# Optimization experiments

Hardware: AMD Instinct MI355X
Metric: run time of the kernel (lower is better)

The kernel has to match this reference:

```python
import jax, jax.numpy as jnp
import numpy as np

B, S, D = 2, 2048, 1024
N_HEADS = 16
HEAD_DIM = D // N_HEADS
D_FF = 4 * D
EPS = 1e-5


def setup_inputs() -> dict:
    key = jax.random.key(0)
    ks = jax.random.split(key, 16)
    s = 0.02
    return {
        "x": jax.random.normal(ks[0], (B, S, D), dtype=jnp.float32),
        "ln1_scale": jnp.ones((D,), jnp.float32),
        "ln1_shift": jnp.zeros((D,), jnp.float32),
        "wq": jax.random.normal(ks[1], (D, D), jnp.float32) * s,
        "wk": jax.random.normal(ks[2], (D, D), jnp.float32) * s,
        "wv": jax.random.normal(ks[3], (D, D), jnp.float32) * s,
        "wo": jax.random.normal(ks[4], (D, D), jnp.float32) * s,
        "bo": jnp.zeros((D,), jnp.float32),
        "ln2_scale": jnp.ones((D,), jnp.float32),
        "ln2_shift": jnp.zeros((D,), jnp.float32),
        "w1": jax.random.normal(ks[5], (D, D_FF), jnp.float32) * s,
        "b1": jnp.zeros((D_FF,), jnp.float32),
        "w2": jax.random.normal(ks[6], (D_FF, D), jnp.float32) * s,
        "b2": jnp.zeros((D,), jnp.float32),
    }


def _layer_norm(x, scale, shift):
    mean = jnp.mean(x, axis=-1, keepdims=True)
    var = jnp.var(x, axis=-1, keepdims=True)  # unbiased=False
    return (x - mean) / jnp.sqrt(var + EPS) * scale + shift


def _mha(x, wq, wk, wv, wo, bo):
    b, s, d = x.shape
    q = (x @ wq).reshape(b, s, N_HEADS, HEAD_DIM).transpose(0, 2, 1, 3)
    k = (x @ wk).reshape(b, s, N_HEADS, HEAD_DIM).transpose(0, 2, 1, 3)
    v = (x @ wv).reshape(b, s, N_HEADS, HEAD_DIM).transpose(0, 2, 1, 3)
    scores = jnp.einsum('bhqd,bhkd->bhqk', q, k)
    causal = jnp.tril(jnp.ones((s, s), dtype=bool))  # mask upper triangle
    scores = jnp.where(causal, scores, -jnp.inf)
    attn = jax.nn.softmax(scores / np.sqrt(HEAD_DIM).astype(np.float32), axis=-1)
    ctx = jnp.einsum('bhqk,bhkd->bhqd', attn, v)
    ctx = ctx.transpose(0, 2, 1, 3).reshape(b, s, d)
    return ctx @ wo + bo


def reference(x, ln1_scale, ln1_shift, wq, wk, wv, wo, bo,
              ln2_scale, ln2_shift, w1, b1, w2, b2):
    # Attention sub-block (dropout is identity in eval / droprate=0)
    h = x + _mha(_layer_norm(x, ln1_scale, ln1_shift), wq, wk, wv, wo, bo)
    # FFN sub-block (note: original code discards the dropout(inp) result and
    # returns shortcut + ff_output, which is the standard residual)
    y = _layer_norm(h, ln2_scale, ln2_shift)
    ff = jax.nn.gelu(y @ w1 + b1, approximate=True) @ w2 + b2
    return h + ff
```

## Files before the change

### kernel.cpp

```cpp
#include <hip/hip_runtime.h>
#include <hip/hip_bf16.h>

typedef unsigned short u16;
typedef unsigned int u32;
typedef __bf16 bf16x8 __attribute__((ext_vector_type(8)));
typedef float f32x4 __attribute__((ext_vector_type(4)));

#if __has_builtin(__builtin_amdgcn_exp2f)
#define FEXP2 __builtin_amdgcn_exp2f
#else
#define FEXP2 exp2f
#endif

#define QSCALE 0.1803368801f

__device__ __forceinline__ u16 f2bf(float f) {
  __hip_bfloat16 h = __float2bfloat16(f);
  return __builtin_bit_cast(u16, h);
}

__device__ __forceinline__ void load_lds16(const u16* g, u16* l) {
  __builtin_amdgcn_global_load_lds((const __attribute__((address_space(1))) void*)g,
                                   (__attribute__((address_space(3))) void*)l, 16, 0, 0);
}

__global__ __launch_bounds__(256) void tconv_kernel(const float* __restrict__ src,
                                                    u16* __restrict__ dst, int R, int C) {
  __shared__ float tile[32][33];
  int bx = blockIdx.x * 32, by = blockIdx.y * 32;
  int tx = threadIdx.x, ty = threadIdx.y;
#pragma unroll
  for (int i = 0; i < 4; ++i)
    tile[ty + 8 * i][tx] = src[(size_t)(by + ty + 8 * i) * C + bx + tx];
  __syncthreads();
#pragma unroll
  for (int i = 0; i < 4; ++i)
    dst[(size_t)(bx + ty + 8 * i) * R + by + tx] = f2bf(tile[tx][ty + 8 * i]);
}

__global__ __launch_bounds__(256) void ln_kernel(const float* __restrict__ src,
                                                 u16* __restrict__ dst,
                                                 const float* __restrict__ gamma,
                                                 const float* __restrict__ beta) {
  int row = blockIdx.x, tid = threadIdx.x;
  const float4 v = ((const float4*)(src + (size_t)row * 1024))[tid];
  float s = v.x + v.y + v.z + v.w;
  float q = v.x * v.x + v.y * v.y + v.z * v.z + v.w * v.w;
#pragma unroll
  for (int off = 32; off >= 1; off >>= 1) {
    s += __shfl_down(s, off, 64);
    q += __shfl_down(q, off, 64);
  }
  __shared__ float red[8];
  if ((tid & 63) == 0) { red[(tid >> 6) * 2] = s; red[(tid >> 6) * 2 + 1] = q; }
  __syncthreads();
  s = red[0] + red[2] + red[4] + red[6];
  q = red[1] + red[3] + red[5] + red[7];
  float mean = s * (1.0f / 1024.0f);
  float var = q * (1.0f / 1024.0f) - mean * mean;
  float rstd = rsqrtf(var + 1e-5f);
  float4 g = ((const float4*)gamma)[tid];
  float4 b = ((const float4*)beta)[tid];
  ushort4 o;
  o.x = f2bf((v.x - mean) * rstd * g.x + b.x);
  o.y = f2bf((v.y - mean) * rstd * g.y + b.y);
  o.z = f2bf((v.z - mean) * rstd * g.z + b.z);
  o.w = f2bf((v.w - mean) * rstd * g.w + b.w);
  *(ushort4*)(dst + (size_t)row * 1024 + tid * 4) = o;
}

template <int MODE, int BN>
__global__ __launch_bounds__(256) void gemm_st(const u16* __restrict__ A,
                                               const u16* __restrict__ BT,
                                               int M, int N, int K,
                                               const float* __restrict__ bias,
                                               const float* __restrict__ resid,
                                               void* __restrict__ outp,
                                               void* __restrict__ outp2,
                                               void* __restrict__ outp3) {
  constexpr int NJ = BN / 32;
  const int tid = threadIdx.x, lane = tid & 63, wave = tid >> 6;
  const int l16 = lane & 15, quad = lane >> 4;
  const int mblk = blockIdx.y * 128, nblk = blockIdx.x * BN;
  const int m0w = (wave >> 1) * 64, n0w = (wave & 1) * (BN / 2);

  __shared__ u16 Ab[128 * 32];
  __shared__ u16 Bb[BN * 32];

  f32x4 acc[4][NJ];
#pragma unroll
  for (int i = 0; i < 4; ++i)
#pragma unroll
    for (int j = 0; j < NJ; ++j)
#pragma unroll
      for (int r = 0; r < 4; ++r) acc[i][j][r] = 0.0f;

  const int srow = lane >> 2, schunk = lane & 3;
  const u16* gA = A + (size_t)(mblk + wave * 32 + srow) * K + schunk * 8;
  u16* lA = Ab + (wave * 32) * 32;
  const u16* gB;
  u16* lB;
  if constexpr (BN == 128) {
    gB = BT + (size_t)(nblk + wave * 32 + srow) * K + schunk * 8;
    lB = Bb + (wave * 32) * 32;
  } else {
    gB = BT + (size_t)(nblk + wave * 16 + srow) * K + schunk * 8;
    lB = Bb + (wave * 16) * 32;
  }

  for (int k0 = 0; k0 < K; k0 += 32) {
    __syncthreads();
    load_lds16(gA + k0, lA);
    load_lds16(gA + 16 * (size_t)K + k0, lA + 16 * 32);
    if constexpr (BN == 128) {
      load_lds16(gB + k0, lB);
      load_lds16(gB + 16 * (size_t)K + k0, lB + 16 * 32);
    } else {
      load_lds16(gB + k0, lB);
    }
    asm volatile("s_waitcnt vmcnt(0)" ::: "memory");
    __syncthreads();

    bf16x8 af[4], bfr[NJ];
#pragma unroll
    for (int i = 0; i < 4; ++i)
      af[i] = *(const bf16x8*)(Ab + (m0w + i * 16 + l16) * 32 + quad * 8);
#pragma unroll
    for (int j = 0; j < NJ; ++j)
      bfr[j] = *(const bf16x8*)(Bb + (n0w + j * 16 + l16) * 32 + quad * 8);
#pragma unroll
    for (int i = 0; i < 4; ++i)
#pragma unroll
      for (int j = 0; j < NJ; ++j)
        acc[i][j] = __builtin_amdgcn_mfma_f32_16x16x32_bf16(af[i], bfr[j], acc[i][j], 0, 0, 0);
  }

#pragma unroll
  for (int i = 0; i < 4; ++i) {
#pragma unroll
    for (int j = 0; j < NJ; ++j) {
      const int col = nblk + n0w + j * 16 + l16;
#pragma unroll
      for (int r = 0; r < 4; ++r) {
        const int row = mblk + m0w + i * 16 + quad * 4 + r;
        float v = acc[i][j][r];
        if constexpr (MODE == 0) {
          const int slotc = col >> 6;
          const int ty = slotc >> 4;
          const int h = slotc & 15, d = col & 63;
          const int bb = row >> 11, s = row & 2047;
          if (ty == 0) {
            ((u16*)outp)[(((size_t)(bb * 16 + h)) * 2048 + s) * 64 + d] = f2bf(v * QSCALE);
          } else if (ty == 1) {
            ((u16*)outp2)[(((size_t)(bb * 16 + h)) * 2048 + s) * 64 + d] = f2bf(v);
          } else {
            const int spos = (s & ~31) | ((s & 15) << 1) | ((s >> 4) & 1);
            ((u16*)outp3)[(((size_t)(bb * 16 + h)) * 64 + d) * 2048 + spos] = f2bf(v);
          }
        } else if constexpr (MODE == 3) {
          ((float*)outp)[(size_t)row * N + col] = v + bias[col] + resid[(size_t)row * N + col];
        } else if constexpr (MODE == 4) {
          float u = v + bias[col];
          float c = 0.7978845608f * u * (1.0f + 0.044715f * u * u);
          float a = fabsf(c);
          float e = __expf(-2.0f * a);
          float th = (1.0f - e) / (1.0f + e);
          th = copysignf(th, c);
          ((u16*)outp)[(size_t)row * N + col] = f2bf(0.5f * u * (1.0f + th));
        } else if constexpr (MODE == 5) {
          ((float*)outp)[(size_t)row * N + col] =
              v + bias[col] + resid[(size_t)row * N + col];
        }
      }
    }
  }
}

__global__ __launch_bounds__(128) void attn_kernel(const u16* __restrict__ Q,
                                                   const u16* __restrict__ Kb,
                                                   const u16* __restrict__ VT,
                                                   u16* __restrict__ ctx) {
  const int tid = threadIdx.x, lane = tid & 63, wave = tid >> 6;
  const int l16 = lane & 15, quad = lane >> 4;
  const int id = blockIdx.x, xcd = id & 7, slot = id >> 3;
  const int bh = xcd + 8 * (slot & 3);
  const int qt = 31 - (slot >> 2);
  const int b = bh >> 4, hh = bh & 15;
  const int q0 = qt * 64 + wave * 32;

  const u16* qp = Q + (size_t)bh * 2048 * 64;
  const u16* kp = Kb + (size_t)bh * 2048 * 64;
  const u16* vp = VT + (size_t)bh * 64 * 2048;

  bf16x8 qf[2][2];
#pragma unroll
  for (int rf = 0; rf < 2; ++rf)
#pragma unroll
    for (int kk = 0; kk < 2; ++kk)
      qf[rf][kk] = *(const bf16x8*)(qp + (size_t)(q0 + rf * 16 + l16) * 64 + kk * 32 + quad * 8);

  f32x4 o[2][4], lac[2];
#pragma unroll
  for (int rf = 0; rf < 2; ++rf) {
#pragma unroll
    for (int r = 0; r < 4; ++r) lac[rf][r] = 0.0f;
#pragma unroll
    for (int dt = 0; dt < 4; ++dt)
#pragma unroll
      for (int r = 0; r < 4; ++r) o[rf][dt][r] = 0.0f;
  }

  bf16x8 onef;
#pragma unroll
  for (int i = 0; i < 8; ++i) onef[i] = (__bf16)1.0f;

  __shared__ u16 pbuf[2][32 * 40];
  u16* pw = pbuf[wave];

  const int nfull = q0 >> 5;

  bf16x8 kf[2][2], vf[4], kfn[2][2], vfn[4];
#pragma unroll
  for (int st = 0; st < 2; ++st)
#pragma unroll
    for (int kk = 0; kk < 2; ++kk)
      kf[st][kk] = *(const bf16x8*)(kp + (size_t)(st * 16 + l16) * 64 + kk * 32 + quad * 8);
#pragma unroll
  for (int dt = 0; dt < 4; ++dt)
    vf[dt] = *(const bf16x8*)(vp + (size_t)(dt * 16 + l16) * 2048 + quad * 8);

  for (int kt = 0; kt <= nfull; ++kt) {
    const int kb0 = kt * 32;
    f32x4 sc[2][2];
#pragma unroll
    for (int rf = 0; rf < 2; ++rf)
#pragma unroll
      for (int st = 0; st < 2; ++st) {
#pragma unroll
        for (int r = 0; r < 4; ++r) sc[rf][st][r] = 0.0f;
#pragma unroll
        for (int kk = 0; kk < 2; ++kk)
          sc[rf][st] = __builtin_amdgcn_mfma_f32_16x16x32_bf16(qf[rf][kk], kf[st][kk], sc[rf][st], 0, 0, 0);
      }

    const int kbn = (kt < nfull) ? kb0 + 32 : 0;
#pragma unroll
    for (int st = 0; st < 2; ++st)
#pragma unroll
      for (int kk = 0; kk < 2; ++kk)
        kfn[st][kk] = *(const bf16x8*)(kp + (size_t)(kbn + st * 16 + l16) * 64 + kk * 32 + quad * 8);
#pragma unroll
    for (int dt = 0; dt < 4; ++dt)
      vfn[dt] = *(const bf16x8*)(vp + (size_t)(dt * 16 + l16) * 2048 + kbn + quad * 8);

    const bool masked = (kt == nfull);
#pragma unroll
    for (int rf = 0; rf < 2; ++rf)
#pragma unroll
      for (int r = 0; r < 4; ++r) {
        float s0 = sc[rf][0][r], s1 = sc[rf][1][r];
        if (masked) {
          const int rel = rf * 16 + quad * 4 + r;
          if (l16 > rel) s0 = -INFINITY;
          if (16 + l16 > rel) s1 = -INFINITY;
        }
        const u32 pk = (u32)f2bf(FEXP2(s0)) | ((u32)f2bf(FEXP2(s1)) << 16);
        *(u32*)(pw + (rf * 16 + quad * 4 + r) * 40 + l16 * 2) = pk;
      }
    asm volatile("s_waitcnt lgkmcnt(0)" ::: "memory");
#pragma unroll
    for (int rf = 0; rf < 2; ++rf) {
      bf16x8 pf = *(const bf16x8*)(pw + (rf * 16 + l16) * 40 + quad * 8);
      lac[rf] = __builtin_amdgcn_mfma_f32_16x16x32_bf16(pf, onef, lac[rf], 0, 0, 0);
#pragma unroll
      for (int dt = 0; dt < 4; ++dt)
        o[rf][dt] = __builtin_amdgcn_mfma_f32_16x16x32_bf16(pf, vf[dt], o[rf][dt], 0, 0, 0);
    }
#pragma unroll
    for (int st = 0; st < 2; ++st)
#pragma unroll
      for (int kk = 0; kk < 2; ++kk) kf[st][kk] = kfn[st][kk];
#pragma unroll
    for (int dt = 0; dt < 4; ++dt) vf[dt] = vfn[dt];
  }

#pragma unroll
  for (int rf = 0; rf < 2; ++rf)
#pragma unroll
    for (int r = 0; r < 4; ++r) {
      const float inv = 1.0f / lac[rf][r];
      const int row = q0 + rf * 16 + quad * 4 + r;
#pragma unroll
      for (int dt = 0; dt < 4; ++dt) {
        const int col = dt * 16 + l16;
        ctx[((size_t)(b * 2048 + row)) * 1024 + hh * 64 + col] = f2bf(o[rf][dt][r] * inv);
      }
    }
}

extern "C" void kernel_launch(void* const* d_in, const int* in_sizes, int n_in,
                              void* d_out, int out_size, void* d_ws, size_t ws_size,
                              hipStream_t stream) {
  (void)in_sizes; (void)n_in; (void)out_size; (void)ws_size;
  const float* x    = (const float*)d_in[0];
  const float* g1   = (const float*)d_in[1];
  const float* s1   = (const float*)d_in[2];
  const float* wq   = (const float*)d_in[3];
  const float* wk   = (const float*)d_in[4];
  const float* wv   = (const float*)d_in[5];
  const float* wo   = (const float*)d_in[6];
  const float* bo   = (const float*)d_in[7];
  const float* g2   = (const float*)d_in[8];
  const float* s2   = (const float*)d_in[9];
  const float* w1   = (const float*)d_in[10];
  const float* b1   = (const float*)d_in[11];
  const float* w2   = (const float*)d_in[12];
  const float* b2   = (const float*)d_in[13];

  char* ws = (char*)d_ws;
  u16* wqkvT = (u16*)(ws + 0);
  u16* woT   = (u16*)(ws + 6291456);
  u16* w1T   = (u16*)(ws + 8388608);
  u16* w2T   = (u16*)(ws + 16777216);
  u16* xn    = (u16*)(ws + 25165824);
  u16* qb    = (u16*)(ws + 33554432);
  u16* kb    = (u16*)(ws + 41943040);
  u16* vT    = (u16*)(ws + 50331648);
  u16* ctx   = (u16*)(ws + 58720256);
  u16* f     = (u16*)(ws + 33554432);
  float* h   = (float*)(ws + 67108864);
  u16* y     = xn;

  dim3 tb(32, 8);
  tconv_kernel<<<dim3(32, 32), tb, 0, stream>>>(wq, wqkvT, 1024, 1024);
  tconv_kernel<<<dim3(32, 32), tb, 0, stream>>>(wk, wqkvT + 1024 * 1024, 1024, 1024);
  tconv_kernel<<<dim3(32, 32), tb, 0, stream>>>(wv, wqkvT + 2048 * 1024, 1024, 1024);
  tconv_kernel<<<dim3(32, 32), tb, 0, stream>>>(wo, woT, 1024, 1024);
  tconv_kernel<<<dim3(128, 32), tb, 0, stream>>>(w1, w1T, 1024, 4096);
  tconv_kernel<<<dim3(32, 128), tb, 0, stream>>>(w2, w2T, 4096, 1024);

  ln_kernel<<<4096, 256, 0, stream>>>(x, xn, g1, s1);

  gemm_st<0, 128><<<dim3(24, 32), 256, 0, stream>>>(xn, wqkvT, 4096, 3072, 1024,
                                                    nullptr, nullptr, qb, kb, vT);

  attn_kernel<<<1024, 128, 0, stream>>>(qb, kb, vT, ctx);

  gemm_st<3, 64><<<dim3(16, 32), 256, 0, stream>>>(ctx, woT, 4096, 1024, 1024, bo, x, h,
                                                   nullptr, nullptr);

  ln_kernel<<<4096, 256, 0, stream>>>(h, y, g2, s2);

  gemm_st<4, 128><<<dim3(32, 32), 256, 0, stream>>>(y, w1T, 4096, 4096, 1024, b1, nullptr, f,
                                                    nullptr, nullptr);
  gemm_st<5, 64><<<dim3(16, 32), 256, 0, stream>>>(f, w2T, 4096, 1024, 4096, b2, h, (float*)d_out,
                                                   nullptr, nullptr);
}
```

Before: 425.6 us.

## Add XCD-aware block remap and a swizzled K64 GEMM for narrow outputs

All GEMMs now use a 1D grid and remap block ids so each XCD handles a contiguous band of M rows, which should improve L2 reuse of A tiles. The two N=1024 projections (attention output and FFN down) move to a new gemm64 kernel. It uses K-step 64 with XOR-swizzled LDS layout to avoid bank conflicts, halves the barrier count per K, and sets launch bounds for two blocks per SM. Epilogue code is factored into a shared helper. Costs are higher LDS use per block and possible register pressure.

```diff
diff --git a/kernel.cpp b/kernel.cpp
--- a/kernel.cpp
+++ b/kernel.cpp
@@ -69,111 +69,187 @@
   *(ushort4*)(dst + (size_t)row * 1024 + tid * 4) = o;
 }
 
-template <int MODE, int BN>
+template <int MODE>
+__device__ __forceinline__ void epilogue_elem(float v, int row, int col, int N,
+                                              const float* __restrict__ bias,
+                                              const float* __restrict__ resid,
+                                              void* __restrict__ outp,
+                                              void* __restrict__ outp2,
+                                              void* __restrict__ outp3) {
+  if constexpr (MODE == 0) {
+    const int slotc = col >> 6;
+    const int ty = slotc >> 4;
+    const int h = slotc & 15, d = col & 63;
+    const int bb = row >> 11, s = row & 2047;
+    if (ty == 0) {
+      ((u16*)outp)[(((size_t)(bb * 16 + h)) * 2048 + s) * 64 + d] = f2bf(v * QSCALE);
+    } else if (ty == 1) {
+      ((u16*)outp2)[(((size_t)(bb * 16 + h)) * 2048 + s) * 64 + d] = f2bf(v);
+    } else {
+      const int spos = (s & ~31) | ((s & 15) << 1) | ((s >> 4) & 1);
+      ((u16*)outp3)[(((size_t)(bb * 16 + h)) * 64 + d) * 2048 + spos] = f2bf(v);
+    }
+  } else if constexpr (MODE == 3) {
+    ((float*)outp)[(size_t)row * N + col] = v + bias[col] + resid[(size_t)row * N + col];
+  } else if constexpr (MODE == 4) {
+    float u = v + bias[col];
+    float c = 0.7978845608f * u * (1.0f + 0.044715f * u * u);
+    float a = fabsf(c);
+    float e = __expf(-2.0f * a);
+    float th = (1.0f - e) / (1.0f + e);
+    th = copysignf(th, c);
+    ((u16*)outp)[(size_t)row * N + col] = f2bf(0.5f * u * (1.0f + th));
+  } else if constexpr (MODE == 5) {
+    ((float*)outp)[(size_t)row * N + col] = v + bias[col] + resid[(size_t)row * N + col];
+  }
+}
+
+template <int MODE>
 __global__ __launch_bounds__(256) void gemm_st(const u16* __restrict__ A,
                                                const u16* __restrict__ BT,
-                                               int M, int N, int K,
+                                               int M, int N, int K, int nbx,
                                                const float* __restrict__ bias,
                                                const float* __restrict__ resid,
                                                void* __restrict__ outp,
                                                void* __restrict__ outp2,
                                                void* __restrict__ outp3) {
-  constexpr int NJ = BN / 32;
   const int tid = threadIdx.x, lane = tid & 63, wave = tid >> 6;
   const int l16 = lane & 15, quad = lane >> 4;
-  const int mblk = blockIdx.y * 128, nblk = blockIdx.x * BN;
-  const int m0w = (wave >> 1) * 64, n0w = (wave & 1) * (BN / 2);
+  const int id = blockIdx.x, xcd = id & 7, s = id >> 3;
+  const int by = xcd * 4 + s / nbx, bx = s - (s / nbx) * nbx;
+  const int mblk = by * 128, nblk = bx * 128;
+  const int m0w = (wave >> 1) * 64, n0w = (wave & 1) * 64;
 
   __shared__ u16 Ab[128 * 32];
-  __shared__ u16 Bb[BN * 32];
-
-  f32x4 acc[4][NJ];
-#pragma unroll
-  for (int i = 0; i < 4; ++i)
-#pragma unroll
-    for (int j = 0; j < NJ; ++j)
+  __shared__ u16 Bb[128 * 32];
+
+  f32x4 acc[4][4];
+#pragma unroll
+  for (int i = 0; i < 4; ++i)
+#pragma unroll
+    for (int j = 0; j < 4; ++j)
 #pragma unroll
       for (int r = 0; r < 4; ++r) acc[i][j][r] = 0.0f;
 
   const int srow = lane >> 2, schunk = lane & 3;
   const u16* gA = A + (size_t)(mblk + wave * 32 + srow) * K + schunk * 8;
   u16* lA = Ab + (wave * 32) * 32;
-  const u16* gB;
-  u16* lB;
-  if constexpr (BN == 128) {
-    gB = BT + (size_t)(nblk + wave * 32 + srow) * K + schunk * 8;
-    lB = Bb + (wave * 32) * 32;
-  } else {
-    gB = BT + (size_t)(nblk + wave * 16 + srow) * K + schunk * 8;
-    lB = Bb + (wave * 16) * 32;
-  }
+  const u16* gB = BT + (size_t)(nblk + wave * 32 + srow) * K + schunk * 8;
+  u16* lB = Bb + (wave * 32) * 32;
 
   for (int k0 = 0; k0 < K; k0 += 32) {
     __syncthreads();
     load_lds16(gA + k0, lA);
     load_lds16(gA + 16 * (size_t)K + k0, lA + 16 * 32);
-    if constexpr (BN == 128) {
-      load_lds16(gB + k0, lB);
-      load_lds16(gB + 16 * (size_t)K + k0, lB + 16 * 32);
-    } else {
-      load_lds16(gB + k0, lB);
-    }
+    load_lds16(gB + k0, lB);
+    load_lds16(gB + 16 * (size_t)K + k0, lB + 16 * 32);
     asm volatile("s_waitcnt vmcnt(0)" ::: "memory");
     __syncthreads();
 
-    bf16x8 af[4], bfr[NJ];
+    bf16x8 af[4], bfr[4];
 #pragma unroll
     for (int i = 0; i < 4; ++i)
       af[i] = *(const bf16x8*)(Ab + (m0w + i * 16 + l16) * 32 + quad * 8);
 #pragma unroll
-    for (int j = 0; j < NJ; ++j)
+    for (int j = 0; j < 4; ++j)
       bfr[j] = *(const bf16x8*)(Bb + (n0w + j * 16 + l16) * 32 + quad * 8);
 #pragma unroll
     for (int i = 0; i < 4; ++i)
 #pragma unroll
-      for (int j = 0; j < NJ; ++j)
+      for (int j = 0; j < 4; ++j)
         acc[i][j] = __builtin_amdgcn_mfma_f32_16x16x32_bf16(af[i], bfr[j], acc[i][j], 0, 0, 0);
   }
 
 #pragma unroll
-  for (int i = 0; i < 4; ++i) {
-#pragma unroll
-    for (int j = 0; j < NJ; ++j) {
+  for (int i = 0; i < 4; ++i)
+#pragma unroll
+    for (int j = 0; j < 4; ++j) {
       const int col = nblk + n0w + j * 16 + l16;
 #pragma unroll
-      for (int r = 0; r < 4; ++r) {
-        const int row = mblk + m0w + i * 16 + quad * 4 + r;
-        float v = acc[i][j][r];
-        if constexpr (MODE == 0) {
-          const int slotc = col >> 6;
-          const int ty = slotc >> 4;
-          const int h = slotc & 15, d = col & 63;
-          const int bb = row >> 11, s = row & 2047;
-          if (ty == 0) {
-            ((u16*)outp)[(((size_t)(bb * 16 + h)) * 2048 + s) * 64 + d] = f2bf(v * QSCALE);
-          } else if (ty == 1) {
-            ((u16*)outp2)[(((size_t)(bb * 16 + h)) * 2048 + s) * 64 + d] = f2bf(v);
-          } else {
-            const int spos = (s & ~31) | ((s & 15) << 1) | ((s >> 4) & 1);
-            ((u16*)outp3)[(((size_t)(bb * 16 + h)) * 64 + d) * 2048 + spos] = f2bf(v);
-          }
-        } else if constexpr (MODE == 3) {
-          ((float*)outp)[(size_t)row * N + col] = v + bias[col] + resid[(size_t)row * N + col];
-        } else if constexpr (MODE == 4) {
-          float u = v + bias[col];
-          float c = 0.7978845608f * u * (1.0f + 0.044715f * u * u);
-          float a = fabsf(c);
-          float e = __expf(-2.0f * a);
-          float th = (1.0f - e) / (1.0f + e);
-          th = copysignf(th, c);
-          ((u16*)outp)[(size_t)row * N + col] = f2bf(0.5f * u * (1.0f + th));
-        } else if constexpr (MODE == 5) {
-          ((float*)outp)[(size_t)row * N + col] =
-              v + bias[col] + resid[(size_t)row * N + col];
-        }
+      for (int r = 0; r < 4; ++r)
+        epilogue_elem<MODE>(acc[i][j][r], mblk + m0w + i * 16 + quad * 4 + r, col, N,
+                            bias, resid, outp, outp2, outp3);
+    }
+}
+
+template <int MODE>
+__global__ __launch_bounds__(256, 2) void gemm64(const u16* __restrict__ A,
+                                                 const u16* __restrict__ BT,
+                                                 int M, int N, int K, int nbx,
+                                                 const float* __restrict__ bias,
+                                                 const float* __restrict__ resid,
+                                                 void* __restrict__ outp) {
+  const int tid = threadIdx.x, lane = tid & 63, wave = tid >> 6;
+  const int l16 = lane & 15, quad = lane >> 4;
+  const int id = blockIdx.x, xcd = id & 7, s = id >> 3;
+  const int by = xcd * 4 + s / nbx, bx = s - (s / nbx) * nbx;
+  const int mblk = by * 128, nblk = bx * 64;
+  const int m0w = (wave >> 1) * 64, n0w = (wave & 1) * 32;
+
+  __shared__ u16 Ab[128 * 64];
+  __shared__ u16 Bb[64 * 64];
+
+  f32x4 acc[4][2];
+#pragma unroll
+  for (int i = 0; i < 4; ++i)
+#pragma unroll
+    for (int j = 0; j < 2; ++j)
+#pragma unroll
+      for (int r = 0; r < 4; ++r) acc[i][j][r] = 0.0f;
+
+  const int lr = lane >> 3, lc = (lane & 7) ^ lr;
+  const u16* gA = A + (size_t)(mblk + wave * 32 + lr) * K + lc * 8;
+  u16* lA = Ab + (wave * 32) * 64;
+  const u16* gB = BT + (size_t)(nblk + wave * 16 + lr) * K + lc * 8;
+  u16* lB = Bb + (wave * 16) * 64;
+
+  const int e = l16 & 7, sl0 = quad ^ e, sl1 = sl0 ^ 4;
+  const u16* pA0 = Ab + (m0w + l16) * 64 + sl0 * 8;
+  const u16* pA1 = Ab + (m0w + l16) * 64 + sl1 * 8;
+  const u16* pB0 = Bb + (n0w + l16) * 64 + sl0 * 8;
+  const u16* pB1 = Bb + (n0w + l16) * 64 + sl1 * 8;
+
+  for (int k0 = 0; k0 < K; k0 += 64) {
+    __syncthreads();
+#pragma unroll
+    for (int t = 0; t < 4; ++t)
+      load_lds16(gA + (size_t)(t * 8) * K + k0, lA + t * 8 * 64);
+#pragma unroll
+    for (int t = 0; t < 2; ++t)
+      load_lds16(gB + (size_t)(t * 8) * K + k0, lB + t * 8 * 64);
+    asm volatile("s_waitcnt vmcnt(0)" ::: "memory");
+    __syncthreads();
+
+    bf16x8 af0[4], af1[4], bf0[2], bf1[2];
+#pragma unroll
+    for (int i = 0; i < 4; ++i) {
+      af0[i] = *(const bf16x8*)(pA0 + i * 16 * 64);
+      af1[i] = *(const bf16x8*)(pA1 + i * 16 * 64);
+    }
+#pragma unroll
+    for (int j = 0; j < 2; ++j) {
+      bf0[j] = *(const bf16x8*)(pB0 + j * 16 * 64);
+      bf1[j] = *(const bf16x8*)(pB1 + j * 16 * 64);
+    }
+#pragma unroll
+    for (int i = 0; i < 4; ++i)
+#pragma unroll
+      for (int j = 0; j < 2; ++j) {
+        acc[i][j] = __builtin_amdgcn_mfma_f32_16x16x32_bf16(af0[i], bf0[j], acc[i][j], 0, 0, 0);
+        acc[i][j] = __builtin_amdgcn_mfma_f32_16x16x32_bf16(af1[i], bf1[j], acc[i][j], 0, 0, 0);
       }
-    }
-  }
+  }
+
+#pragma unroll
+  for (int i = 0; i < 4; ++i)
+#pragma unroll
+    for (int j = 0; j < 2; ++j) {
+      const int col = nblk + n0w + j * 16 + l16;
+#pragma unroll
+      for (int r = 0; r < 4; ++r)
+        epilogue_elem<MODE>(acc[i][j][r], mblk + m0w + i * 16 + quad * 4 + r, col, N,
+                            bias, resid, outp, nullptr, nullptr);
+    }
 }
 
 __global__ __launch_bounds__(128) void attn_kernel(const u16* __restrict__ Q,
@@ -341,18 +417,16 @@
 
   ln_kernel<<<4096, 256, 0, stream>>>(x, xn, g1, s1);
 
-  gemm_st<0, 128><<<dim3(24, 32), 256, 0, stream>>>(xn, wqkvT, 4096, 3072, 1024,
-                                                    nullptr, nullptr, qb, kb, vT);
+  gemm_st<0><<<768, 256, 0, stream>>>(xn, wqkvT, 4096, 3072, 1024, 24,
+                                      nullptr, nullptr, qb, kb, vT);
 
   attn_kernel<<<1024, 128, 0, stream>>>(qb, kb, vT, ctx);
 
-  gemm_st<3, 64><<<dim3(16, 32), 256, 0, stream>>>(ctx, woT, 4096, 1024, 1024, bo, x, h,
-                                                   nullptr, nullptr);
+  gemm64<3><<<512, 256, 0, stream>>>(ctx, woT, 4096, 1024, 1024, 16, bo, x, h);
 
   ln_kernel<<<4096, 256, 0, stream>>>(h, y, g2, s2);
 
-  gemm_st<4, 128><<<dim3(32, 32), 256, 0, stream>>>(y, w1T, 4096, 4096, 1024, b1, nullptr, f,
-                                                    nullptr, nullptr);
-  gemm_st<5, 64><<<dim3(16, 32), 256, 0, stream>>>(f, w2T, 4096, 1024, 4096, b2, h, (float*)d_out,
-                                                   nullptr, nullptr);
-}
+  gemm_st<4><<<1024, 256, 0, stream>>>(y, w1T, 4096, 4096, 1024, 32,
+                                       b1, nullptr, f, nullptr, nullptr);
+  gemm64<5><<<512, 256, 0, stream>>>(f, w2T, 4096, 1024, 4096, 16, b2, h, (float*)d_out);
+}
```

Result: faster. 400.6 us (-5.9%).
